# Kernel optimization log

Hardware: AMD Instinct MI355X
Metric: run time of the kernel (lower is better)

Reference implementation:

```python
import jax, jax.numpy as jnp
import numpy as np
import math

IN_SIZE = 512
OUT_SIZE = 512
N_HEADS = 8
D_K = OUT_SIZE // N_HEADS  # 64
N_NTYPES = 4
N_ETYPES = 8
MAX_LEN = 240
E = 150000


def _sinusoid_table():
    # RelTemporalEncoding fixed (non-trainable) embedding table [MAX_LEN, IN_SIZE]
    position = np.arange(0.0, MAX_LEN, dtype=np.float64)[:, None]
    div_term = np.exp(np.arange(0, IN_SIZE, 2, dtype=np.float64) * -(math.log(10000.0) / IN_SIZE))
    emb = np.zeros((MAX_LEN, IN_SIZE), dtype=np.float64)
    emb[:, 0::2] = np.sin(position * div_term) / IN_SIZE ** 0.5
    emb[:, 1::2] = np.cos(position * div_term) / IN_SIZE ** 0.5
    return jnp.asarray(emb, dtype=jnp.float32)


def typed_linear(x, types, W, b=None):
    """x: [E, ..., in], types: int[E], W: [T, out, in], b: [T, out] or None.
    Small fixed loop over T types with masked accumulation (avoids gathering a
    huge [E, out, in] weight tensor)."""
    out = jnp.zeros(x.shape[:-1] + (W.shape[1],), x.dtype)
    t_exp = types.reshape((-1,) + (1,) * (x.ndim - 1))
    for t in range(W.shape[0]):
        y = jnp.einsum('...i,oi->...o', x, W[t])
        if b is not None:
            y = y + b[t]
        out = out + jnp.where(t_exp == t, y, jnp.zeros((), x.dtype))
    return out


def setup_inputs() -> dict:
    key = jax.random.key(0)
    ks = jax.random.split(key, 12)
    xavier = lambda k, shape, fan_in, fan_out: jax.random.uniform(
        k, shape, jnp.float32, -1.0, 1.0) * math.sqrt(6.0 / (fan_in + fan_out))
    inp = {
        'h_s': jax.random.normal(ks[0], (E, IN_SIZE), jnp.float32),
        'Q_t': jax.random.normal(ks[1], (E, N_HEADS, D_K), jnp.float32),
        'etype': jax.random.randint(ks[2], (E,), 0, N_ETYPES),
        'tau_s': jax.random.randint(ks[3], (E,), 0, N_NTYPES),
        'dt': jax.random.randint(ks[4], (E,), 0, MAX_LEN),
        # RelTemporalEncoding params
        'emb': _sinusoid_table(),  # fixed, non-trainable
        'lin_W': xavier(ks[5], (IN_SIZE, IN_SIZE), IN_SIZE, IN_SIZE),
        'lin_b': jnp.zeros((IN_SIZE,), jnp.float32),
        # TypedLinear params (xavier_uniform like the torch code)
        'K_W': xavier(ks[6], (N_NTYPES, OUT_SIZE, IN_SIZE), IN_SIZE, OUT_SIZE),
        'K_b': jnp.zeros((N_NTYPES, OUT_SIZE), jnp.float32),
        'V_W': xavier(ks[7], (N_NTYPES, OUT_SIZE, IN_SIZE), IN_SIZE, OUT_SIZE),
        'V_b': jnp.zeros((N_NTYPES, OUT_SIZE), jnp.float32),
        'Watt_W': xavier(ks[8], (N_ETYPES, D_K, D_K), D_K, D_K),
        'Wmsg_W': xavier(ks[9], (N_ETYPES, D_K, D_K), D_K, D_K),
        'mu': jnp.ones((N_ETYPES, N_HEADS), jnp.float32),
    }
    return inp


def reference(h_s, Q_t, etype, tau_s, dt, emb, lin_W, lin_b,
              K_W, K_b, V_W, V_b, Watt_W, Wmsg_W, mu):
    n_edges = h_s.shape[0]
    # RelTemporalEncoding: x + Linear(emb[t])
    h_hat = h_s + emb[dt] @ lin_W.T + lin_b  # [E, in]
    # Typed K/V projections by source node type
    K_s = typed_linear(h_hat, tau_s, K_W, K_b).reshape(n_edges, N_HEADS, D_K)
    V_s = typed_linear(h_hat, tau_s, V_W, V_b).reshape(n_edges, N_HEADS, D_K)
    # Typed per-edge-type transforms
    M = typed_linear(V_s, etype, Wmsg_W)          # [E, H, d_k]
    att_head_k = typed_linear(K_s, etype, Watt_W)  # [E, H, d_k]
    att_head = (Q_t * att_head_k).sum(-1)          # [E, H]
    att_head = att_head * mu[etype] / D_K ** 0.5
    return att_head, M
```

## Files before the change

kernel.cpp:

```cpp
#include <hip/hip_runtime.h>
#include <hip/hip_bf16.h>
#include <stdint.h>

#define E_N 150000
#define IN 512
#define HEADS 8
#define DK 64
#define MAXLEN 240

#define PT 150272
#define PE 150528

typedef __attribute__((ext_vector_type(8))) short short8;
typedef __attribute__((ext_vector_type(4))) short short4v;
typedef __attribute__((ext_vector_type(4))) float f32x4;

#define OFF_R    0UL
#define OFF_WC   491520UL
#define OFF_BIAS 4685824UL
#define OFF_CNT  4702208UL
#define OFF_PT   4702464UL
#define OFF_PE   5303552UL
#define OFF_KS   5905664UL

static __device__ __forceinline__ short f2bf(float f) {
  union { float f; uint32_t u; } v; v.f = f;
  uint32_t u = v.u;
  uint32_t r = (u + 0x7fffu + ((u >> 16) & 1u)) >> 16;
  return (short)r;
}

__global__ __launch_bounds__(256) void k_rte(const float* __restrict__ emb,
    const float* __restrict__ linW, const float* __restrict__ linB,
    float* __restrict__ R) {
  __shared__ float x[IN];
  int p = blockIdx.x;
  for (int i = threadIdx.x; i < IN; i += 256) x[i] = emb[p * IN + i];
  __syncthreads();
  for (int o = threadIdx.x; o < IN; o += 256) {
    const float* w = linW + (long)o * IN;
    float s = 0.f;
#pragma unroll 4
    for (int k = 0; k < IN; k += 4) {
      float4 wv = *(const float4*)(w + k);
      s += wv.x * x[k] + wv.y * x[k + 1] + wv.z * x[k + 2] + wv.w * x[k + 3];
    }
    R[p * IN + o] = s + linB[o];
  }
}

__global__ __launch_bounds__(256) void k_cvtw(const float* __restrict__ KW,
    const float* __restrict__ VW, short* __restrict__ Wc) {
  long idx = ((long)blockIdx.x * 256 + threadIdx.x) * 4;
  int t = (int)(idx >> 19);
  int rem = (int)(idx & ((1 << 19) - 1));
  int o = rem >> 9;
  int k = rem & 511;
  const float* src = (o < 512) ? (KW + ((long)(t * 512 + o) * 512) + k)
                               : (VW + ((long)(t * 512 + (o - 512)) * 512) + k);
  float4 v = *(const float4*)src;
  short4v b;
  b.x = f2bf(v.x); b.y = f2bf(v.y); b.z = f2bf(v.z); b.w = f2bf(v.w);
  *(short4v*)(Wc + idx) = b;
}

__global__ __launch_bounds__(256) void k_cvtb(const float* __restrict__ Kb,
    const float* __restrict__ Vb, float* __restrict__ biasC) {
  int idx = blockIdx.x * 256 + threadIdx.x;
  int t = idx >> 10;
  int o = idx & 1023;
  biasC[idx] = (o < 512) ? Kb[t * 512 + o] : Vb[t * 512 + (o - 512)];
}

__global__ __launch_bounds__(256) void k_hist(const int* __restrict__ tau,
    const int* __restrict__ et, int* __restrict__ cnt) {
  __shared__ int l[12];
  if (threadIdx.x < 12) l[threadIdx.x] = 0;
  __syncthreads();
  int e = blockIdx.x * 256 + threadIdx.x;
  if (e < E_N) {
    atomicAdd(&l[tau[e]], 1);
    atomicAdd(&l[4 + et[e]], 1);
  }
  __syncthreads();
  if (threadIdx.x < 12) atomicAdd(&cnt[threadIdx.x], l[threadIdx.x]);
}

__global__ void k_bases(int* c) {
  int b = 0;
  for (int t = 0; t < 4; t++) { c[12 + t] = b; b += ((c[t] + 63) >> 6) << 6; }
  b = 0;
  for (int g = 0; g < 8; g++) { c[16 + g] = b; b += ((c[4 + g] + 63) >> 6) << 6; }
  for (int i = 24; i < 36; i++) c[i] = 0;
}

__global__ __launch_bounds__(256) void k_scatter(const int* __restrict__ tau,
    const int* __restrict__ et, int* __restrict__ c,
    int* __restrict__ permT, int* __restrict__ permE) {
  __shared__ int lc[12], lbase[12];
  if (threadIdx.x < 12) lc[threadIdx.x] = 0;
  __syncthreads();
  int e = blockIdx.x * 256 + threadIdx.x;
  bool v = e < E_N;
  int t = 0, g = 0, pt = 0, pe = 0;
  if (v) {
    t = tau[e]; g = et[e];
    pt = atomicAdd(&lc[t], 1);
    pe = atomicAdd(&lc[4 + g], 1);
  }
  __syncthreads();
  if (threadIdx.x < 12) {
    int n = lc[threadIdx.x];
    int base = 0;
    if (n > 0) {
      if (threadIdx.x < 4) base = atomicAdd(&c[24 + threadIdx.x], n);
      else                 base = atomicAdd(&c[28 + (threadIdx.x - 4)], n);
    }
    lbase[threadIdx.x] = base;
  }
  __syncthreads();
  if (v) {
    permT[c[12 + t] + lbase[t] + pt] = e;
    permE[c[16 + g] + lbase[4 + g] + pe] = e;
  }
}

__global__ __launch_bounds__(512, 1) void k_gemm(
    const float* __restrict__ hs, const float* __restrict__ R,
    const int* __restrict__ dt, const int* __restrict__ tau,
    const short* __restrict__ Wc, const float* __restrict__ biasC,
    const int* __restrict__ perm,
    short* __restrict__ Ks, float* Mout) {
  __shared__ short sA[64][40];
  __shared__ int eRow[64];
  __shared__ int dtRow[64];
  __shared__ int metaT;
  int tid = threadIdx.x;
  int m0 = blockIdx.x * 64;
  if (tid < 64) {
    int e = perm[m0 + tid];
    eRow[tid] = e;
    dtRow[tid] = (e >= 0) ? dt[e] : 0;
  }
  __syncthreads();
  if (tid == 0) {
    int t = -1;
    for (int i = 0; i < 64; i++)
      if (eRow[i] >= 0) { t = tau[eRow[i]]; break; }
    metaT = t;
  }
  __syncthreads();
  int t = metaT;
  if (t < 0) return;

  int lane = tid & 63;
  int wv = tid >> 6;
  int oWave = wv * 128;
  int l15 = lane & 15;
  int lk8 = (lane >> 4) * 8;

  f32x4 acc[4][8] = {};

  int srow = tid >> 3;
  int skq = (tid & 7) * 4;
  int sE = eRow[srow];
  const float* hsrc = hs + (long)(sE >= 0 ? sE : 0) * IN + skq;
  const float* rsrc = R + (long)dtRow[srow] * IN + skq;

  const short* wbase = Wc + ((long)t * 1024 + oWave + l15) * IN + lk8;

  float4 hv = {0, 0, 0, 0}, rv = {0, 0, 0, 0};
  if (sE >= 0) { hv = *(const float4*)hsrc; rv = *(const float4*)rsrc; }

  for (int kk = 0; kk < 16; kk++) {
    int k0 = kk * 32;
    short4v sv;
    sv.x = f2bf(hv.x + rv.x);
    sv.y = f2bf(hv.y + rv.y);
    sv.z = f2bf(hv.z + rv.z);
    sv.w = f2bf(hv.w + rv.w);
    *(short4v*)&sA[srow][skq] = sv;
    if (kk < 15 && sE >= 0) {
      hv = *(const float4*)(hsrc + (kk + 1) * 32);
      rv = *(const float4*)(rsrc + (kk + 1) * 32);
    }
    __syncthreads();
    short8 a[4], b[8];
#pragma unroll
    for (int mi = 0; mi < 4; mi++)
      a[mi] = *(const short8*)&sA[mi * 16 + l15][lk8];
#pragma unroll
    for (int ni = 0; ni < 8; ni++)
      b[ni] = *(const short8*)(wbase + (long)ni * 16 * IN + k0);
#pragma unroll
    for (int mi = 0; mi < 4; mi++)
#pragma unroll
      for (int ni = 0; ni < 8; ni++)
        acc[mi][ni] = __builtin_amdgcn_mfma_f32_16x16x32_bf16(a[mi], b[ni], acc[mi][ni], 0, 0, 0);
    __syncthreads();
  }

  int rbase = (lane >> 4) * 4;
  float bias[8];
#pragma unroll
  for (int ni = 0; ni < 8; ni++)
    bias[ni] = biasC[t * 1024 + oWave + ni * 16 + l15];
#pragma unroll
  for (int mi = 0; mi < 4; mi++) {
#pragma unroll
    for (int r = 0; r < 4; r++) {
      int row = mi * 16 + rbase + r;
      int e = eRow[row];
      if (e < 0) continue;
      short* vdst = (short*)((char*)Mout + (size_t)e * 2048 + 1024);
#pragma unroll
      for (int ni = 0; ni < 8; ni++) {
        int col = oWave + ni * 16 + l15;
        float v = acc[mi][ni][r] + bias[ni];
        if (col < 512) Ks[(long)e * IN + col] = f2bf(v);
        else           vdst[col - 512] = f2bf(v);
      }
    }
  }
}

__global__ __launch_bounds__(512, 1) void k_stage2(
    const int* __restrict__ perm, const int* __restrict__ et,
    const float* __restrict__ WattW, const float* __restrict__ WmsgW,
    const float* __restrict__ Qt, const float* __restrict__ mu,
    const short* __restrict__ Ks, float* Mout,
    float* __restrict__ attOut) {
  __shared__ short Wm[64][68];
  __shared__ short Wa[64][68];
  __shared__ float muL[8];
  __shared__ int eArr[64];
  __shared__ int metaG;
  int tid = threadIdx.x;
  int m0 = blockIdx.x * 64;
  if (tid < 64) eArr[tid] = perm[m0 + tid];
  __syncthreads();
  if (tid == 0) {
    int g = -1;
    for (int i = 0; i < 64; i++)
      if (eArr[i] >= 0) { g = et[eArr[i]]; break; }
    metaG = g;
  }
  __syncthreads();
  int g = metaG;
  if (g < 0) return;

  for (int i = tid; i < 4096; i += 512) {
    int o = i >> 6, k = i & 63;
    Wm[o][k] = f2bf(WmsgW[(long)g * 4096 + i]);
    Wa[o][k] = f2bf(WattW[(long)g * 4096 + i]);
  }
  if (tid < 8) muL[tid] = mu[g * 8 + tid];
  __syncthreads();

  int lane = tid & 63;
  int wv = tid >> 6;
  int wvBase = wv * 64;
  int l15 = lane & 15;
  int lk8 = (lane >> 4) * 8;
  int rbase = (lane >> 4) * 4;

  int eA[4], hA[4];
#pragma unroll
  for (int mi = 0; mi < 4; mi++) {
    int lr = wvBase + mi * 16 + l15;
    int e = eArr[lr >> 3];
    eA[mi] = (e >= 0) ? e : 0;
    hA[mi] = lr & 7;
  }

  {
    short8 av[4][2];
#pragma unroll
    for (int mi = 0; mi < 4; mi++) {
      const short* vp = (const short*)((const char*)Mout + (size_t)eA[mi] * 2048 + 1024)
                        + hA[mi] * 64 + lk8;
      av[mi][0] = *(const short8*)vp;
      av[mi][1] = *(const short8*)(vp + 32);
    }
    short8 bm[4][2];
#pragma unroll
    for (int ni = 0; ni < 4; ni++)
#pragma unroll
      for (int kk = 0; kk < 2; kk++)
        bm[ni][kk] = *(const short8*)&Wm[ni * 16 + l15][kk * 32 + lk8];
    f32x4 accM[4][4] = {};
#pragma unroll
    for (int kk = 0; kk < 2; kk++)
#pragma unroll
      for (int mi = 0; mi < 4; mi++)
#pragma unroll
        for (int ni = 0; ni < 4; ni++)
          accM[mi][ni] = __builtin_amdgcn_mfma_f32_16x16x32_bf16(av[mi][kk], bm[ni][kk], accM[mi][ni], 0, 0, 0);
#pragma unroll
    for (int mi = 0; mi < 4; mi++) {
#pragma unroll
      for (int r = 0; r < 4; r++) {
        int lr = wvBase + mi * 16 + rbase + r;
        int e = eArr[lr >> 3];
        if (e < 0) continue;
        int h = lr & 7;
#pragma unroll
        for (int ni = 0; ni < 4; ni++)
          Mout[(long)e * 512 + h * 64 + ni * 16 + l15] = accM[mi][ni][r];
      }
    }
  }

  {
    short8 ak[4][2];
#pragma unroll
    for (int mi = 0; mi < 4; mi++) {
      const short* kp = Ks + (long)eA[mi] * 512 + hA[mi] * 64 + lk8;
      ak[mi][0] = *(const short8*)kp;
      ak[mi][1] = *(const short8*)(kp + 32);
    }
    short8 ba[4][2];
#pragma unroll
    for (int ni = 0; ni < 4; ni++)
#pragma unroll
      for (int kk = 0; kk < 2; kk++)
        ba[ni][kk] = *(const short8*)&Wa[ni * 16 + l15][kk * 32 + lk8];
    f32x4 accA[4][4] = {};
#pragma unroll
    for (int kk = 0; kk < 2; kk++)
#pragma unroll
      for (int mi = 0; mi < 4; mi++)
#pragma unroll
        for (int ni = 0; ni < 4; ni++)
          accA[mi][ni] = __builtin_amdgcn_mfma_f32_16x16x32_bf16(ak[mi][kk], ba[ni][kk], accA[mi][ni], 0, 0, 0);
#pragma unroll
    for (int mi = 0; mi < 4; mi++) {
#pragma unroll
      for (int r = 0; r < 4; r++) {
        int lr = wvBase + mi * 16 + rbase + r;
        int e = eArr[lr >> 3];
        if (e < 0) continue;
        int h = lr & 7;
        const float* qp = Qt + ((long)e * 8 + h) * 64 + l15;
        float s = 0.f;
#pragma unroll
        for (int ni = 0; ni < 4; ni++)
          s += qp[ni * 16] * accA[mi][ni][r];
        s += __shfl_xor(s, 1);
        s += __shfl_xor(s, 2);
        s += __shfl_xor(s, 4);
        s += __shfl_xor(s, 8);
        if (l15 == 0) attOut[(long)e * 8 + h] = s * muL[h] * 0.125f;
      }
    }
  }
}

extern "C" void kernel_launch(void* const* d_in, const int* in_sizes, int n_in,
                              void* d_out, int out_size, void* d_ws, size_t ws_size,
                              hipStream_t stream) {
  const float* hs    = (const float*)d_in[0];
  const float* Qt    = (const float*)d_in[1];
  const int*   et    = (const int*)d_in[2];
  const int*   tau   = (const int*)d_in[3];
  const int*   dt    = (const int*)d_in[4];
  const float* emb   = (const float*)d_in[5];
  const float* linW  = (const float*)d_in[6];
  const float* linB  = (const float*)d_in[7];
  const float* KW    = (const float*)d_in[8];
  const float* Kb    = (const float*)d_in[9];
  const float* VW    = (const float*)d_in[10];
  const float* Vb    = (const float*)d_in[11];
  const float* WattW = (const float*)d_in[12];
  const float* WmsgW = (const float*)d_in[13];
  const float* mu    = (const float*)d_in[14];

  char* ws = (char*)d_ws;
  float* R     = (float*)(ws + OFF_R);
  short* Wc    = (short*)(ws + OFF_WC);
  float* biasC = (float*)(ws + OFF_BIAS);
  int*   cnt   = (int*)(ws + OFF_CNT);
  int*   permT = (int*)(ws + OFF_PT);
  int*   permE = (int*)(ws + OFF_PE);
  short* Ks    = (short*)(ws + OFF_KS);

  float* attOut = (float*)d_out;
  float* Mout   = (float*)d_out + (long)E_N * 8;

  hipMemsetAsync(cnt, 0, 64 * sizeof(int), stream);
  hipMemsetAsync(permT, 0xFF, PT * sizeof(int), stream);
  hipMemsetAsync(permE, 0xFF, PE * sizeof(int), stream);

  k_rte<<<240, 256, 0, stream>>>(emb, linW, linB, R);
  k_cvtw<<<2048, 256, 0, stream>>>(KW, VW, Wc);
  k_cvtb<<<16, 256, 0, stream>>>(Kb, Vb, biasC);
  k_hist<<<(E_N + 255) / 256, 256, 0, stream>>>(tau, et, cnt);
  k_bases<<<1, 1, 0, stream>>>(cnt);
  k_scatter<<<(E_N + 255) / 256, 256, 0, stream>>>(tau, et, cnt, permT, permE);
  k_gemm<<<PT / 64, 512, 0, stream>>>(hs, R, dt, tau, Wc, biasC, permT, Ks, Mout);
  k_stage2<<<PE / 64, 512, 0, stream>>>(permE, et, WattW, WmsgW, Qt, mu, Ks, Mout, attOut);
}
```

Measured before the change: 807.0 us.

## Precompute bf16 h_hat and retile typed GEMM with direct-to-LDS loads

A new kernel computes h_hat = h_s + R[dt] in bf16 once per edge and stages it in the unused half of the output buffer. The typed K/V GEMM now uses 128x128 tiles, is split over eight output-column tiles with a block-index swizzle, and loads both A and the weights through global_load_lds into swizzled LDS. Previously each block streamed the weights straight from global memory into registers at one block per CU. The second stage is split into separate message and attention kernels, and the type lookup now reads only the first edge of each tile. The cost is an extra pass over memory to write and reread the bf16 h_hat, plus one more kernel launch.

Result: faster. 693.3 us (-14.1%).

```diff
diff --git a/kernel.cpp b/kernel.cpp
--- a/kernel.cpp
+++ b/kernel.cpp
@@ -4,12 +4,11 @@
 
 #define E_N 150000
 #define IN 512
-#define HEADS 8
-#define DK 64
 #define MAXLEN 240
 
-#define PT 150272
+#define PT 150528
 #define PE 150528
+#define NTILE_T 1176
 
 typedef __attribute__((ext_vector_type(8))) short short8;
 typedef __attribute__((ext_vector_type(4))) short short4v;
@@ -20,8 +19,8 @@
 #define OFF_BIAS 4685824UL
 #define OFF_CNT  4702208UL
 #define OFF_PT   4702464UL
-#define OFF_PE   5303552UL
-#define OFF_KS   5905664UL
+#define OFF_PE   5304576UL
+#define OFF_KS   5906688UL
 
 static __device__ __forceinline__ short f2bf(float f) {
   union { float f; uint32_t u; } v; v.f = f;
@@ -88,7 +87,7 @@
 
 __global__ void k_bases(int* c) {
   int b = 0;
-  for (int t = 0; t < 4; t++) { c[12 + t] = b; b += ((c[t] + 63) >> 6) << 6; }
+  for (int t = 0; t < 4; t++) { c[12 + t] = b; b += ((c[t] + 127) >> 7) << 7; }
   b = 0;
   for (int g = 0; g < 8; g++) { c[16 + g] = b; b += ((c[4 + g] + 63) >> 6) << 6; }
   for (int i = 24; i < 36; i++) c[i] = 0;
@@ -125,112 +124,202 @@
   }
 }
 
-__global__ __launch_bounds__(512, 1) void k_gemm(
-    const float* __restrict__ hs, const float* __restrict__ R,
-    const int* __restrict__ dt, const int* __restrict__ tau,
+__global__ __launch_bounds__(256) void k_hhat(const float* __restrict__ hs,
+    const float* __restrict__ R, const int* __restrict__ dt,
+    char* __restrict__ out) {
+  int tid = threadIdx.x;
+  long e = (long)blockIdx.x * 16 + (tid >> 4);
+  int sub = tid & 15;
+  const float* hp = hs + e * 512 + sub * 32;
+  const float* rp = R + (long)dt[e] * 512 + sub * 32;
+  short* op = (short*)(out + e * 2048) + sub * 32;
+#pragma unroll
+  for (int j = 0; j < 4; j++) {
+    float4 h0 = *(const float4*)(hp + j * 8);
+    float4 h1 = *(const float4*)(hp + j * 8 + 4);
+    float4 r0 = *(const float4*)(rp + j * 8);
+    float4 r1 = *(const float4*)(rp + j * 8 + 4);
+    short8 o;
+    o[0] = f2bf(h0.x + r0.x); o[1] = f2bf(h0.y + r0.y);
+    o[2] = f2bf(h0.z + r0.z); o[3] = f2bf(h0.w + r0.w);
+    o[4] = f2bf(h1.x + r1.x); o[5] = f2bf(h1.y + r1.y);
+    o[6] = f2bf(h1.z + r1.z); o[7] = f2bf(h1.w + r1.w);
+    *(short8*)(op + j * 8) = o;
+  }
+}
+
+__global__ __launch_bounds__(256, 4) void k_gemm(
+    const char* __restrict__ hhat,
+    const int* __restrict__ tau,
     const short* __restrict__ Wc, const float* __restrict__ biasC,
     const int* __restrict__ perm,
     short* __restrict__ Ks, float* Mout) {
-  __shared__ short sA[64][40];
-  __shared__ int eRow[64];
-  __shared__ int dtRow[64];
+  __shared__ short sA[4096];
+  __shared__ short sB[4096];
+  __shared__ int eRow[128];
   __shared__ int metaT;
   int tid = threadIdx.x;
-  int m0 = blockIdx.x * 64;
-  if (tid < 64) {
-    int e = perm[m0 + tid];
-    eRow[tid] = e;
-    dtRow[tid] = (e >= 0) ? dt[e] : 0;
-  }
-  __syncthreads();
+  int l = (blockIdx.x & 7) * NTILE_T + (blockIdx.x >> 3);
+  int ttile = l >> 3, ctile = l & 7;
+  int m0 = ttile * 128;
+  if (tid < 128) eRow[tid] = perm[m0 + tid];
   if (tid == 0) {
-    int t = -1;
-    for (int i = 0; i < 64; i++)
-      if (eRow[i] >= 0) { t = tau[eRow[i]]; break; }
-    metaT = t;
+    int e0 = perm[m0];
+    metaT = (e0 >= 0) ? tau[e0] : -1;
   }
   __syncthreads();
   int t = metaT;
   if (t < 0) return;
+  int n0 = ctile * 128;
+
+  int lane = tid & 63;
+  int w = tid >> 6;
+  int wm = w >> 1, wn = w & 1;
+
+  int rS = w * 32 + (lane >> 2);
+  int cS = lane & 3;
+  int e0r = eRow[rS];      if (e0r < 0) e0r = 0;
+  int e1r = eRow[rS + 16]; if (e1r < 0) e1r = 0;
+  int ch0 = (cS - (rS >> 1)) & 3;
+  int ch1 = (cS - ((rS + 16) >> 1)) & 3;
+  const char* srcA0 = hhat + (size_t)e0r * 2048 + ch0 * 16;
+  const char* srcA1 = hhat + (size_t)e1r * 2048 + ch1 * 16;
+  const char* wcb = (const char*)(Wc + ((size_t)t * 1024 + n0) * 512);
+  const char* srcB0 = wcb + (size_t)rS * 1024 + ch0 * 16;
+  const char* srcB1 = wcb + (size_t)(rS + 16) * 1024 + ch1 * 16;
+  char* dA0 = (char*)sA + w * 2048;
+  char* dA1 = (char*)sA + w * 2048 + 1024;
+  char* dB0 = (char*)sB + w * 2048;
+  char* dB1 = (char*)sB + w * 2048 + 1024;
+
+  int aRow = wm * 64 + (lane & 15);
+  int aOff = aRow * 64 + ((((lane >> 4) + (aRow >> 1)) & 3) << 4);
+  int bRow = wn * 64 + (lane & 15);
+  int bOff = bRow * 64 + ((((lane >> 4) + (bRow >> 1)) & 3) << 4);
+
+  f32x4 acc[4][4] = {};
+#pragma unroll
+  for (int kk = 0; kk < 16; kk++) {
+    __syncthreads();
+    __builtin_amdgcn_global_load_lds((const uint32_t*)(srcA0 + kk * 64), (uint32_t*)dA0, 16, 0, 0);
+    __builtin_amdgcn_global_load_lds((const uint32_t*)(srcA1 + kk * 64), (uint32_t*)dA1, 16, 0, 0);
+    __builtin_amdgcn_global_load_lds((const uint32_t*)(srcB0 + kk * 64), (uint32_t*)dB0, 16, 0, 0);
+    __builtin_amdgcn_global_load_lds((const uint32_t*)(srcB1 + kk * 64), (uint32_t*)dB1, 16, 0, 0);
+    __syncthreads();
+    short8 a[4], b[4];
+#pragma unroll
+    for (int mi = 0; mi < 4; mi++)
+      a[mi] = *(const short8*)((const char*)sA + aOff + mi * 1024);
+#pragma unroll
+    for (int ni = 0; ni < 4; ni++)
+      b[ni] = *(const short8*)((const char*)sB + bOff + ni * 1024);
+#pragma unroll
+    for (int mi = 0; mi < 4; mi++)
+#pragma unroll
+      for (int ni = 0; ni < 4; ni++)
+        acc[mi][ni] = __builtin_amdgcn_mfma_f32_16x16x32_bf16(a[mi], b[ni], acc[mi][ni], 0, 0, 0);
+  }
+
+  int l15 = lane & 15;
+  int rbase = (lane >> 4) * 4;
+  bool isK = ctile < 4;
+  float bias[4];
+#pragma unroll
+  for (int ni = 0; ni < 4; ni++)
+    bias[ni] = biasC[t * 1024 + n0 + wn * 64 + ni * 16 + l15];
+#pragma unroll
+  for (int mi = 0; mi < 4; mi++) {
+#pragma unroll
+    for (int r = 0; r < 4; r++) {
+      int row = wm * 64 + mi * 16 + rbase + r;
+      int e = eRow[row];
+      if (e < 0) continue;
+      if (isK) {
+        short* kd = Ks + (size_t)e * 512 + n0 + wn * 64;
+#pragma unroll
+        for (int ni = 0; ni < 4; ni++)
+          kd[ni * 16 + l15] = f2bf(acc[mi][ni][r] + bias[ni]);
+      } else {
+        short* vd = (short*)((char*)Mout + (size_t)e * 2048 + 1024) + (n0 - 512) + wn * 64;
+#pragma unroll
+        for (int ni = 0; ni < 4; ni++)
+          vd[ni * 16 + l15] = f2bf(acc[mi][ni][r] + bias[ni]);
+      }
+    }
+  }
+}
+
+__global__ __launch_bounds__(512, 1) void k_msg(
+    const int* __restrict__ perm, const int* __restrict__ et,
+    const float* __restrict__ WmsgW, float* Mout) {
+  __shared__ short Wm[64][68];
+  __shared__ int eArr[64];
+  __shared__ int metaG;
+  int tid = threadIdx.x;
+  int m0 = blockIdx.x * 64;
+  if (tid < 64) eArr[tid] = perm[m0 + tid];
+  if (tid == 0) {
+    int e0 = perm[m0];
+    metaG = (e0 >= 0) ? et[e0] : -1;
+  }
+  __syncthreads();
+  int g = metaG;
+  if (g < 0) return;
+  for (int i = tid; i < 4096; i += 512)
+    Wm[i >> 6][i & 63] = f2bf(WmsgW[(long)g * 4096 + i]);
+  __syncthreads();
 
   int lane = tid & 63;
   int wv = tid >> 6;
-  int oWave = wv * 128;
+  int wvBase = wv * 64;
   int l15 = lane & 15;
   int lk8 = (lane >> 4) * 8;
-
-  f32x4 acc[4][8] = {};
-
-  int srow = tid >> 3;
-  int skq = (tid & 7) * 4;
-  int sE = eRow[srow];
-  const float* hsrc = hs + (long)(sE >= 0 ? sE : 0) * IN + skq;
-  const float* rsrc = R + (long)dtRow[srow] * IN + skq;
-
-  const short* wbase = Wc + ((long)t * 1024 + oWave + l15) * IN + lk8;
-
-  float4 hv = {0, 0, 0, 0}, rv = {0, 0, 0, 0};
-  if (sE >= 0) { hv = *(const float4*)hsrc; rv = *(const float4*)rsrc; }
-
-  for (int kk = 0; kk < 16; kk++) {
-    int k0 = kk * 32;
-    short4v sv;
-    sv.x = f2bf(hv.x + rv.x);
-    sv.y = f2bf(hv.y + rv.y);
-    sv.z = f2bf(hv.z + rv.z);
-    sv.w = f2bf(hv.w + rv.w);
-    *(short4v*)&sA[srow][skq] = sv;
-    if (kk < 15 && sE >= 0) {
-      hv = *(const float4*)(hsrc + (kk + 1) * 32);
-      rv = *(const float4*)(rsrc + (kk + 1) * 32);
+  int rbase = (lane >> 4) * 4;
+
+  short8 av[4][2];
+#pragma unroll
+  for (int mi = 0; mi < 4; mi++) {
+    int lr = wvBase + mi * 16 + l15;
+    int e = eArr[lr >> 3]; if (e < 0) e = 0;
+    const short* vp = (const short*)((const char*)Mout + (size_t)e * 2048 + 1024)
+                      + (lr & 7) * 64 + lk8;
+    av[mi][0] = *(const short8*)vp;
+    av[mi][1] = *(const short8*)(vp + 32);
+  }
+  short8 bm[4][2];
+#pragma unroll
+  for (int ni = 0; ni < 4; ni++)
+#pragma unroll
+    for (int kk = 0; kk < 2; kk++)
+      bm[ni][kk] = *(const short8*)&Wm[ni * 16 + l15][kk * 32 + lk8];
+  f32x4 accM[4][4] = {};
+#pragma unroll
+  for (int kk = 0; kk < 2; kk++)
+#pragma unroll
+    for (int mi = 0; mi < 4; mi++)
+#pragma unroll
+      for (int ni = 0; ni < 4; ni++)
+        accM[mi][ni] = __builtin_amdgcn_mfma_f32_16x16x32_bf16(av[mi][kk], bm[ni][kk], accM[mi][ni], 0, 0, 0);
+#pragma unroll
+  for (int mi = 0; mi < 4; mi++) {
+#pragma unroll
+    for (int r = 0; r < 4; r++) {
+      int lr = wvBase + mi * 16 + rbase + r;
+      int e = eArr[lr >> 3];
+      if (e < 0) continue;
+      int h = lr & 7;
+#pragma unroll
+      for (int ni = 0; ni < 4; ni++)
+        Mout[(long)e * 512 + h * 64 + ni * 16 + l15] = accM[mi][ni][r];
     }
-    __syncthreads();
-    short8 a[4], b[8];
-#pragma unroll
-    for (int mi = 0; mi < 4; mi++)
-      a[mi] = *(const short8*)&sA[mi * 16 + l15][lk8];
-#pragma unroll
-    for (int ni = 0; ni < 8; ni++)
-      b[ni] = *(const short8*)(wbase + (long)ni * 16 * IN + k0);
-#pragma unroll
-    for (int mi = 0; mi < 4; mi++)
-#pragma unroll
-      for (int ni = 0; ni < 8; ni++)
-        acc[mi][ni] = __builtin_amdgcn_mfma_f32_16x16x32_bf16(a[mi], b[ni], acc[mi][ni], 0, 0, 0);
-    __syncthreads();
-  }
-
-  int rbase = (lane >> 4) * 4;
-  float bias[8];
-#pragma unroll
-  for (int ni = 0; ni < 8; ni++)
-    bias[ni] = biasC[t * 1024 + oWave + ni * 16 + l15];
-#pragma unroll
-  for (int mi = 0; mi < 4; mi++) {
-#pragma unroll
-    for (int r = 0; r < 4; r++) {
-      int row = mi * 16 + rbase + r;
-      int e = eRow[row];
-      if (e < 0) continue;
-      short* vdst = (short*)((char*)Mout + (size_t)e * 2048 + 1024);
-#pragma unroll
-      for (int ni = 0; ni < 8; ni++) {
-        int col = oWave + ni * 16 + l15;
-        float v = acc[mi][ni][r] + bias[ni];
-        if (col < 512) Ks[(long)e * IN + col] = f2bf(v);
-        else           vdst[col - 512] = f2bf(v);
-      }
-    }
-  }
-}
-
-__global__ __launch_bounds__(512, 1) void k_stage2(
+  }
+}
+
+__global__ __launch_bounds__(512, 1) void k_att(
     const int* __restrict__ perm, const int* __restrict__ et,
-    const float* __restrict__ WattW, const float* __restrict__ WmsgW,
-    const float* __restrict__ Qt, const float* __restrict__ mu,
-    const short* __restrict__ Ks, float* Mout,
+    const float* __restrict__ WattW, const float* __restrict__ Qt,
+    const float* __restrict__ mu, const short* __restrict__ Ks,
     float* __restrict__ attOut) {
-  __shared__ short Wm[64][68];
   __shared__ short Wa[64][68];
   __shared__ float muL[8];
   __shared__ int eArr[64];
@@ -238,22 +327,15 @@
   int tid = threadIdx.x;
   int m0 = blockIdx.x * 64;
   if (tid < 64) eArr[tid] = perm[m0 + tid];
-  __syncthreads();
   if (tid == 0) {
-    int g = -1;
-    for (int i = 0; i < 64; i++)
-      if (eArr[i] >= 0) { g = et[eArr[i]]; break; }
-    metaG = g;
+    int e0 = perm[m0];
+    metaG = (e0 >= 0) ? et[e0] : -1;
   }
   __syncthreads();
   int g = metaG;
   if (g < 0) return;
-
-  for (int i = tid; i < 4096; i += 512) {
-    int o = i >> 6, k = i & 63;
-    Wm[o][k] = f2bf(WmsgW[(long)g * 4096 + i]);
-    Wa[o][k] = f2bf(WattW[(long)g * 4096 + i]);
-  }
+  for (int i = tid; i < 4096; i += 512)
+    Wa[i >> 6][i & 63] = f2bf(WattW[(long)g * 4096 + i]);
   if (tid < 8) muL[tid] = mu[g * 8 + tid];
   __syncthreads();
 
@@ -264,94 +346,47 @@
   int lk8 = (lane >> 4) * 8;
   int rbase = (lane >> 4) * 4;
 
-  int eA[4], hA[4];
+  short8 ak[4][2];
 #pragma unroll
   for (int mi = 0; mi < 4; mi++) {
     int lr = wvBase + mi * 16 + l15;
-    int e = eArr[lr >> 3];
-    eA[mi] = (e >= 0) ? e : 0;
-    hA[mi] = lr & 7;
-  }
-
-  {
-    short8 av[4][2];
-#pragma unroll
-    for (int mi = 0; mi < 4; mi++) {
-      const short* vp = (const short*)((const char*)Mout + (size_t)eA[mi] * 2048 + 1024)
-                        + hA[mi] * 64 + lk8;
-      av[mi][0] = *(const short8*)vp;
-      av[mi][1] = *(const short8*)(vp + 32);
-    }
-    short8 bm[4][2];
-#pragma unroll
-    for (int ni = 0; ni < 4; ni++)
-#pragma unroll
-      for (int kk = 0; kk < 2; kk++)
-        bm[ni][kk] = *(const short8*)&Wm[ni * 16 + l15][kk * 32 + lk8];
-    f32x4 accM[4][4] = {};
+    int e = eArr[lr >> 3]; if (e < 0) e = 0;
+    const short* kp = Ks + (size_t)e * 512 + (lr & 7) * 64 + lk8;
+    ak[mi][0] = *(const short8*)kp;
+    ak[mi][1] = *(const short8*)(kp + 32);
+  }
+  short8 ba[4][2];
+#pragma unroll
+  for (int ni = 0; ni < 4; ni++)
 #pragma unroll
     for (int kk = 0; kk < 2; kk++)
-#pragma unroll
-      for (int mi = 0; mi < 4; mi++)
-#pragma unroll
-        for (int ni = 0; ni < 4; ni++)
-          accM[mi][ni] = __builtin_amdgcn_mfma_f32_16x16x32_bf16(av[mi][kk], bm[ni][kk], accM[mi][ni], 0, 0, 0);
-#pragma unroll
-    for (int mi = 0; mi < 4; mi++) {
-#pragma unroll
-      for (int r = 0; r < 4; r++) {
-        int lr = wvBase + mi * 16 + rbase + r;
-        int e = eArr[lr >> 3];
-        if (e < 0) continue;
-        int h = lr & 7;
-#pragma unroll
-        for (int ni = 0; ni < 4; ni++)
-          Mout[(long)e * 512 + h * 64 + ni * 16 + l15] = accM[mi][ni][r];
-      }
-    }
-  }
-
-  {
-    short8 ak[4][2];
-#pragma unroll
-    for (int mi = 0; mi < 4; mi++) {
-      const short* kp = Ks + (long)eA[mi] * 512 + hA[mi] * 64 + lk8;
-      ak[mi][0] = *(const short8*)kp;
-      ak[mi][1] = *(const short8*)(kp + 32);
-    }
-    short8 ba[4][2];
-#pragma unroll
-    for (int ni = 0; ni < 4; ni++)
-#pragma unroll
-      for (int kk = 0; kk < 2; kk++)
-        ba[ni][kk] = *(const short8*)&Wa[ni * 16 + l15][kk * 32 + lk8];
-    f32x4 accA[4][4] = {};
-#pragma unroll
-    for (int kk = 0; kk < 2; kk++)
-#pragma unroll
-      for (int mi = 0; mi < 4; mi++)
-#pragma unroll
-        for (int ni = 0; ni < 4; ni++)
-          accA[mi][ni] = __builtin_amdgcn_mfma_f32_16x16x32_bf16(ak[mi][kk], ba[ni][kk], accA[mi][ni], 0, 0, 0);
-#pragma unroll
-    for (int mi = 0; mi < 4; mi++) {
-#pragma unroll
-      for (int r = 0; r < 4; r++) {
-        int lr = wvBase + mi * 16 + rbase + r;
-        int e = eArr[lr >> 3];
-        if (e < 0) continue;
-        int h = lr & 7;
-        const float* qp = Qt + ((long)e * 8 + h) * 64 + l15;
-        float s = 0.f;
-#pragma unroll
-        for (int ni = 0; ni < 4; ni++)
-          s += qp[ni * 16] * accA[mi][ni][r];
-        s += __shfl_xor(s, 1);
-        s += __shfl_xor(s, 2);
-        s += __shfl_xor(s, 4);
-        s += __shfl_xor(s, 8);
-        if (l15 == 0) attOut[(long)e * 8 + h] = s * muL[h] * 0.125f;
-      }
+      ba[ni][kk] = *(const short8*)&Wa[ni * 16 + l15][kk * 32 + lk8];
+  f32x4 accA[4][4] = {};
+#pragma unroll
+  for (int kk = 0; kk < 2; kk++)
+#pragma unroll
+    for (int mi = 0; mi < 4; mi++)
+#pragma unroll
+      for (int ni = 0; ni < 4; ni++)
+        accA[mi][ni] = __builtin_amdgcn_mfma_f32_16x16x32_bf16(ak[mi][kk], ba[ni][kk], accA[mi][ni], 0, 0, 0);
+#pragma unroll
+  for (int mi = 0; mi < 4; mi++) {
+#pragma unroll
+    for (int r = 0; r < 4; r++) {
+      int lr = wvBase + mi * 16 + rbase + r;
+      int e = eArr[lr >> 3];
+      if (e < 0) continue;
+      int h = lr & 7;
+      const float* qp = Qt + ((long)e * 8 + h) * 64 + l15;
+      float s = 0.f;
+#pragma unroll
+      for (int ni = 0; ni < 4; ni++)
+        s += qp[ni * 16] * accA[mi][ni][r];
+      s += __shfl_xor(s, 1);
+      s += __shfl_xor(s, 2);
+      s += __shfl_xor(s, 4);
+      s += __shfl_xor(s, 8);
+      if (l15 == 0) attOut[(long)e * 8 + h] = s * muL[h] * 0.125f;
     }
   }
 }
@@ -397,6 +432,8 @@
   k_hist<<<(E_N + 255) / 256, 256, 0, stream>>>(tau, et, cnt);
   k_bases<<<1, 1, 0, stream>>>(cnt);
   k_scatter<<<(E_N + 255) / 256, 256, 0, stream>>>(tau, et, cnt, permT, permE);
-  k_gemm<<<PT / 64, 512, 0, stream>>>(hs, R, dt, tau, Wc, biasC, permT, Ks, Mout);
-  k_stage2<<<PE / 64, 512, 0, stream>>>(permE, et, WattW, WmsgW, Qt, mu, Ks, Mout, attOut);
-}
+  k_hhat<<<E_N / 16, 256, 0, stream>>>(hs, R, dt, (char*)Mout);
+  k_gemm<<<NTILE_T * 8, 256, 0, stream>>>((const char*)Mout, tau, Wc, biasC, permT, Ks, Mout);
+  k_msg<<<PE / 64, 512, 0, stream>>>(permE, et, WmsgW, Mout);
+  k_att<<<PE / 64, 512, 0, stream>>>(permE, et, WattW, Qt, mu, Ks, attOut);
+}
```
